# Performance work log

Measured on AMD Instinct MI355X. Metric: run time of the kernel, lower is better.

## Reference

```python
import jax
import jax.numpy as jnp
import numpy as np

ALPHA = 0.95
NUM_POS_FREQS = 4
CROSS_WEIGHT = 0.5
TOPK = 16
EPS = 1e-12


def _pos_enc(coords):
    # coords: [N, 4] -> [N, 4 * 2 * NUM_POS_FREQS]
    N = coords.shape[0]
    freqs = 2.0 ** jnp.arange(NUM_POS_FREQS, dtype=coords.dtype)  # [F]
    angles = coords[:, :, None] * (2.0 * jnp.pi) * freqs          # [N,4,F]
    pe = jnp.concatenate([jnp.sin(angles), jnp.cos(angles)], axis=-1)  # [N,4,2F]
    return pe.reshape(N, -1)


def _cosine_sim(x, y):
    # row-wise cosine similarity: [N,C] x [M,C] -> [N,M]
    xn = x / jnp.maximum(jnp.linalg.norm(x, axis=-1, keepdims=True), EPS)
    yn = y / jnp.maximum(jnp.linalg.norm(y, axis=-1, keepdims=True), EPS)
    return xn @ yn.T


def _sparsify_topk(A, k):
    # row-wise top-k, self-loop always kept (diag forced to max before top-k)
    N = A.shape[0]
    diag = jnp.arange(N)
    A_with_self = A.at[diag, diag].set(jnp.finfo(A.dtype).max)
    _, topk_idx = jax.lax.top_k(A_with_self, k)                   # [N,k]
    mask = jnp.zeros(A.shape, dtype=bool).at[diag[:, None], topk_idx].set(True)
    return jnp.where(mask, A, jnp.zeros((), A.dtype))


def _sym_normalize(A):
    deg = jnp.clip(A.sum(axis=-1, keepdims=True), EPS, None)      # [N,1]
    d_inv_sqrt = deg ** -0.5
    return d_inv_sqrt * A * d_inv_sqrt.T


def _build_adjacency(features, coordinates, history_features, history_coords):
    B, C = features.shape
    n, K, _ = history_features.shape
    H = n * K

    cur_feats = features
    cur_pos = _pos_enc(coordinates)
    A_cur = ALPHA * _cosine_sim(cur_feats, cur_feats) + (1.0 - ALPHA) * _cosine_sim(cur_pos, cur_pos)

    hist_feats = history_features.reshape(H, C)
    hist_pos = _pos_enc(history_coords.reshape(H, 4))
    A_hist = ALPHA * _cosine_sim(hist_feats, hist_feats) + (1.0 - ALPHA) * _cosine_sim(hist_pos, hist_pos)

    A_cross = ALPHA * _cosine_sim(cur_feats, hist_feats) + (1.0 - ALPHA) * _cosine_sim(cur_pos, hist_pos)
    A_cross = CROSS_WEIGHT * A_cross

    A = jnp.block([[A_cur, A_cross], [A_cross.T, A_hist]])        # [N,N], N=B+H
    node_feats = jnp.concatenate([cur_feats, hist_feats], axis=0)

    N = A.shape[0]
    if TOPK is not None and TOPK < N:
        A = _sparsify_topk(A, TOPK)
    A = _sym_normalize(A)
    return A[None], node_feats[None]


def setup_inputs() -> dict:
    key = jax.random.key(0)
    k1, k2, k3, k4 = jax.random.split(key, 4)
    B, C, n, K = 4096, 256, 128, 32
    return {
        "features": jax.random.normal(k1, (B, C), dtype=jnp.float32),
        "coordinates": jax.random.uniform(k2, (B, 4), dtype=jnp.float32),
        "history_features": jax.random.normal(k3, (n, K, C), dtype=jnp.float32),
        "history_coords": jax.random.uniform(k4, (n, K, 4), dtype=jnp.float32),
    }


def reference(features, coordinates, history_features, history_coords):
    adj, node_feats = _build_adjacency(features, coordinates, history_features, history_coords)
    return adj, node_feats
```

## Files before the change

### kernel.cpp

```cpp
#include <hip/hip_runtime.h>
#include <math.h>

#define B_CUR 4096
#define N_TOT 8192
#define C_F   256
#define C_TOT 288
#define KSEL  16

typedef unsigned short u16;
typedef __attribute__((ext_vector_type(8))) short short8;
typedef __attribute__((ext_vector_type(4))) float floatx4;

__device__ inline float bf2f(u16 v) {
  union { unsigned int u; float f; } x; x.u = ((unsigned int)v) << 16; return x.f;
}
__device__ inline u16 f2bf(float f) {
  union { float f; unsigned int u; } x; x.f = f;
  unsigned int u = x.u;
  u += ((u >> 16) & 1u) + 0x7FFFu;
  return (u16)(u >> 16);
}

#define GLD_LDS16(g, l) __builtin_amdgcn_global_load_lds(                      \
    (const __attribute__((address_space(1))) unsigned int*)(g),                \
    (__attribute__((address_space(3))) unsigned int*)(l), 16, 0, 0)

__global__ __launch_bounds__(256) void k_prep_feats(
    const float* __restrict__ feats, const float* __restrict__ hfeats,
    u16* __restrict__ Zb, float* __restrict__ out_nf) {
  int wave = threadIdx.x >> 6;
  int lane = threadIdx.x & 63;
  int row  = blockIdx.x * 4 + wave;
  const float* src = (row < B_CUR) ? (feats + (size_t)row * C_F)
                                   : (hfeats + (size_t)(row - B_CUR) * C_F);
  int c0 = lane * 4;
  float4 raw = *(const float4*)(src + c0);
  float ss = raw.x*raw.x + raw.y*raw.y + raw.z*raw.z + raw.w*raw.w;
  #pragma unroll
  for (int m = 32; m; m >>= 1) ss += __shfl_xor(ss, m, 64);
  float scale = 0.97467943448089633f / fmaxf(sqrtf(ss), 1e-12f);
  ushort4 o;
  o.x = f2bf(raw.x*scale); o.y = f2bf(raw.y*scale);
  o.z = f2bf(raw.z*scale); o.w = f2bf(raw.w*scale);
  *(ushort4*)(Zb + (size_t)row * C_TOT + c0) = o;
  *(float4*)(out_nf + (size_t)row * C_F + c0) = raw;
}

__global__ void k_prep_pos(const float* __restrict__ coords,
                           const float* __restrict__ hcoords,
                           u16* __restrict__ Zb) {
  int r = blockIdx.x * blockDim.x + threadIdx.x;
  if (r >= N_TOT) return;
  const float* src = (r < B_CUR) ? (coords + (size_t)r * 4)
                                 : (hcoords + (size_t)(r - B_CUR) * 4);
  float pe[32];
  float ss = 0.f;
  #pragma unroll
  for (int d = 0; d < 4; ++d) {
    float base = src[d] * 6.283185307179586f;
    #pragma unroll
    for (int f = 0; f < 4; ++f) {
      float ang = base * (float)(1 << f);
      float s = sinf(ang), co = cosf(ang);
      pe[d*8 + f]     = s;
      pe[d*8 + 4 + f] = co;
      ss += s*s + co*co;
    }
  }
  float scale = 0.22360679774997896f / fmaxf(sqrtf(ss), 1e-12f);
  u16* dst = Zb + (size_t)r * C_TOT + C_F;
  #pragma unroll
  for (int k = 0; k < 32; ++k) dst[k] = f2bf(pe[k] * scale);
}

#define EP_STRIDE 136
__global__ __launch_bounds__(256) void k_gemm_mfma(const u16* __restrict__ Zb,
                                                   u16* __restrict__ adj16) {
  __shared__ __align__(16) u16 smem[128 * EP_STRIDE];
  u16* As = smem;
  u16* Bs = smem + 4096;
  int tid  = threadIdx.x;
  int bi   = blockIdx.y, bj = blockIdx.x;
  int wave = tid >> 6, lane = tid & 63;
  int quad = lane >> 4, l16 = lane & 15;
  int m0w  = (wave >> 1) * 64;
  int n0w  = (wave & 1) * 64;
  int i0   = bi * 128, j0 = bj * 128;

  floatx4 acc[4][4];
  #pragma unroll
  for (int a = 0; a < 4; ++a)
    #pragma unroll
    for (int b = 0; b < 4; ++b) acc[a][b] = (floatx4){0.f, 0.f, 0.f, 0.f};

  int srow = wave * 16 + (lane >> 2);
  int sseg = (lane & 3) * 8;
  for (int kt = 0; kt < C_TOT; kt += 32) {
    #pragma unroll
    for (int it = 0; it < 2; ++it) {
      int row = it * 64 + srow;
      const u16* ga = Zb + (size_t)(i0 + row) * C_TOT + kt + sseg;
      const u16* gb = Zb + (size_t)(j0 + row) * C_TOT + kt + sseg;
      GLD_LDS16(ga, As + (it * 64 + wave * 16) * 32 + lane * 8);
      GLD_LDS16(gb, Bs + (it * 64 + wave * 16) * 32 + lane * 8);
    }
    __builtin_amdgcn_s_waitcnt(0);
    __syncthreads();
    short8 af[4], bf[4];
    #pragma unroll
    for (int mi = 0; mi < 4; ++mi)
      af[mi] = *(const short8*)(&As[(m0w + mi*16 + l16) * 32 + quad * 8]);
    #pragma unroll
    for (int ni = 0; ni < 4; ++ni)
      bf[ni] = *(const short8*)(&Bs[(n0w + ni*16 + l16) * 32 + quad * 8]);
    #pragma unroll
    for (int mi = 0; mi < 4; ++mi)
      #pragma unroll
      for (int ni = 0; ni < 4; ++ni)
        acc[mi][ni] = __builtin_amdgcn_mfma_f32_16x16x32_bf16(
            af[mi], bf[ni], acc[mi][ni], 0, 0, 0);
    __syncthreads();
  }

  float w = ((bi < 32) != (bj < 32)) ? 0.5f : 1.0f;
  #pragma unroll
  for (int mi = 0; mi < 4; ++mi) {
    #pragma unroll
    for (int ni = 0; ni < 4; ++ni) {
      int col = n0w + ni * 16 + l16;
      #pragma unroll
      for (int rg = 0; rg < 4; ++rg) {
        int row = m0w + mi * 16 + quad * 4 + rg;
        smem[row * EP_STRIDE + col] = f2bf(acc[mi][ni][rg] * w);
      }
    }
  }
  __syncthreads();
  #pragma unroll
  for (int it = 0; it < 8; ++it) {
    int idx = it * 256 + tid;
    int row = idx >> 4, l = idx & 15;
    uint4 v = *(const uint4*)(&smem[row * EP_STRIDE + l * 8]);
    *(uint4*)(&adj16[(size_t)(i0 + row) * 16384 + j0 + l * 8]) = v;
  }
}

#define TOP2(x) { unsigned int xv_ = (x); \
  if (xv_ > m1) { m2 = m1; m1 = xv_; } else if (xv_ > m2) { m2 = xv_; } }

__global__ __launch_bounds__(256) void k_topk(
    const u16* __restrict__ adj16,
    int* __restrict__ topk_idx, float* __restrict__ topk_val,
    float* __restrict__ deg_out) {
  __shared__ unsigned int keys[N_TOT];
  __shared__ unsigned int cand[64];
  __shared__ float s_diag;
  int r = blockIdx.x;
  int t = threadIdx.x;
  int wave = t >> 6, lane = t & 63;
  const u16* rowp = adj16 + (size_t)r * 16384;

  #pragma unroll
  for (int it = 0; it < 4; ++it) {
    int c0 = it * 2048 + t * 8;
    uint4 v = *(const uint4*)(rowp + c0);
    u16 e[8]; *(uint4*)e = v;
    unsigned int kk[8];
    #pragma unroll
    for (int q = 0; q < 8; ++q) {
      unsigned int b = e[q];
      unsigned int s16 = (b & 0x8000u) ? (b ^ 0xFFFFu) : (b | 0x8000u);
      kk[q] = (s16 << 16) | (unsigned int)(8191 - (c0 + q));
    }
    *(uint4*)(&keys[c0])     = *(uint4*)(&kk[0]);
    *(uint4*)(&keys[c0 + 4]) = *(uint4*)(&kk[4]);
  }
  __syncthreads();
  if (t == 0) {
    s_diag = bf2f(rowp[r]);
    keys[r] = 0xFFFF0000u | (unsigned int)(8191 - r);
  }
  __syncthreads();
  float diagval = s_diag;

  unsigned int m1 = 0, m2 = 0;
  int base = wave * 2048 + lane * 4;
  #pragma unroll
  for (int j = 0; j < 8; ++j) {
    uint4 v = *(const uint4*)(&keys[base + j * 256]);
    TOP2(v.x) TOP2(v.y) TOP2(v.z) TOP2(v.w)
  }

  for (int it = 0; it < KSEL; ++it) {
    unsigned int wmax = m1;
    #pragma unroll
    for (int s = 32; s; s >>= 1) {
      unsigned int o = (unsigned int)__shfl_xor((int)wmax, s, 64);
      wmax = (o > wmax) ? o : wmax;
    }
    if (lane == it) cand[wave * 16 + it] = wmax;
    if (m1 == wmax) {
      int col = 8191 - (int)(wmax & 0x1FFFu);
      keys[col] = 0;
      if (m2 != 0) { m1 = m2; m2 = 0; }
      else {
        m1 = 0; m2 = 0;
        #pragma unroll
        for (int j = 0; j < 8; ++j) {
          uint4 v = *(const uint4*)(&keys[base + j * 256]);
          TOP2(v.x) TOP2(v.y) TOP2(v.z) TOP2(v.w)
        }
      }
    }
  }
  __syncthreads();

  if (wave == 0) {
    unsigned int c = cand[lane];
    unsigned int myWin = 0;
    for (int it = 0; it < KSEL; ++it) {
      unsigned int wmax = c;
      #pragma unroll
      for (int s = 32; s; s >>= 1) {
        unsigned int o = (unsigned int)__shfl_xor((int)wmax, s, 64);
        wmax = (o > wmax) ? o : wmax;
      }
      if (c == wmax) c = 0;
      if (lane == it) myWin = wmax;
    }
    float val = 0.f;
    int col = 0;
    if (lane < KSEL) {
      unsigned int p = myWin;
      col = 8191 - (int)(p & 0x1FFFu);
      unsigned int k16 = p >> 16;
      unsigned int b = (k16 & 0x8000u) ? (k16 ^ 0x8000u) : ((~k16) & 0xFFFFu);
      val = (col == r) ? diagval : bf2f((u16)b);
      topk_idx[r * KSEL + lane] = col;
      topk_val[r * KSEL + lane] = val;
    }
    float s = (lane < KSEL) ? val : 0.f;
    #pragma unroll
    for (int m = 8; m; m >>= 1) s += __shfl_xor(s, m, 64);
    if (lane == 0) deg_out[r] = s;
  }
}

__global__ __launch_bounds__(256) void k_scale_zero(
    float* __restrict__ adj, const int* __restrict__ topk_idx,
    const float* __restrict__ topk_val, const float* __restrict__ deg) {
  int r = blockIdx.x, t = threadIdx.x;
  float* row = adj + (size_t)r * N_TOT;
  const float4 z4 = make_float4(0.f, 0.f, 0.f, 0.f);
  #pragma unroll
  for (int kk = 0; kk < 8; ++kk)
    *(float4*)(row + kk * 1024 + t * 4) = z4;
  __syncthreads();
  if (t < KSEL) {
    int j = topk_idx[r * KSEL + t];
    if (j < 0) j = 0; if (j >= N_TOT) j = N_TOT - 1;
    float v = topk_val[r * KSEL + t];
    float di = 1.0f / sqrtf(fmaxf(deg[r], 1e-12f));
    float dj = 1.0f / sqrtf(fmaxf(deg[j], 1e-12f));
    row[j] = v * di * dj;
  }
}

extern "C" void kernel_launch(void* const* d_in, const int* in_sizes, int n_in,
                              void* d_out, int out_size, void* d_ws, size_t ws_size,
                              hipStream_t stream) {
  const float* feats   = (const float*)d_in[0];
  const float* coords  = (const float*)d_in[1];
  const float* hfeats  = (const float*)d_in[2];
  const float* hcoords = (const float*)d_in[3];
  float* out    = (float*)d_out;
  float* adj    = out;
  u16*   adj16  = (u16*)out;
  float* out_nf = out + (size_t)N_TOT * N_TOT;

  char* ws    = (char*)d_ws;
  u16*  Zb    = (u16*)ws;
  size_t zb   = (size_t)N_TOT * C_TOT * sizeof(u16);
  zb = (zb + 255) & ~(size_t)255;
  int*   t_idx = (int*)(ws + zb);
  float* t_val = (float*)(ws + zb + (size_t)N_TOT*KSEL*sizeof(int));
  float* deg   = (float*)(ws + zb + (size_t)N_TOT*KSEL*(sizeof(int)+sizeof(float)));

  hipLaunchKernelGGL(k_prep_feats, dim3(N_TOT/4), dim3(256), 0, stream,
                     feats, hfeats, Zb, out_nf);
  hipLaunchKernelGGL(k_prep_pos, dim3(N_TOT/256), dim3(256), 0, stream,
                     coords, hcoords, Zb);
  hipLaunchKernelGGL(k_gemm_mfma, dim3(64, 64), dim3(256), 0, stream, Zb, adj16);
  hipLaunchKernelGGL(k_topk, dim3(N_TOT), dim3(256), 0, stream,
                     adj16, t_idx, t_val, deg);
  hipLaunchKernelGGL(k_scale_zero, dim3(N_TOT), dim3(256), 0, stream,
                     adj, t_idx, t_val, deg);
}
```

Measured before the change: 436.9 us.

## Exploit symmetry in Gram GEMM and widen K-tile to 96

The GEMM now launches only upper-triangular 128x128 tiles, decoding the tile index with a sqrt-based formula, and writes each off-diagonal tile twice, once directly and once transposed through shared memory. This roughly halves the MFMA work and the operand loads, since the similarity matrix is symmetric. The K loop also stages 96 columns per iteration instead of 32, cutting barrier and waitcnt round-trips at the cost of more LDS per block (48KB). Extra costs are a second epilogue pass with a column-major LDS write, which may hit bank conflicts, and uneven grid sizing.

```diff
diff --git a/kernel.cpp b/kernel.cpp
--- a/kernel.cpp
+++ b/kernel.cpp
@@ -6,6 +6,7 @@
 #define C_F   256
 #define C_TOT 288
 #define KSEL  16
+#define NTILE 64
 
 typedef unsigned short u16;
 typedef __attribute__((ext_vector_type(8))) short short8;
@@ -76,11 +77,19 @@
 #define EP_STRIDE 136
 __global__ __launch_bounds__(256) void k_gemm_mfma(const u16* __restrict__ Zb,
                                                    u16* __restrict__ adj16) {
-  __shared__ __align__(16) u16 smem[128 * EP_STRIDE];
+  __shared__ __align__(16) u16 smem[2 * 128 * 96];
   u16* As = smem;
-  u16* Bs = smem + 4096;
+  u16* Bs = smem + 128 * 96;
   int tid  = threadIdx.x;
-  int bi   = blockIdx.y, bj = blockIdx.x;
+
+  int t = blockIdx.x;
+  int bi = (int)floorf(((2.0f*NTILE + 1.0f) -
+            sqrtf((float)((2*NTILE+1)*(2*NTILE+1)) - 8.0f*(float)t)) * 0.5f);
+  if (bi < 0) bi = 0; if (bi > NTILE-1) bi = NTILE-1;
+  while (bi > 0 && t < bi*NTILE - bi*(bi-1)/2) --bi;
+  while (bi < NTILE-1 && t >= (bi+1)*NTILE - (bi+1)*bi/2) ++bi;
+  int bj = bi + (t - (bi*NTILE - bi*(bi-1)/2));
+
   int wave = tid >> 6, lane = tid & 63;
   int quad = lane >> 4, l16 = lane & 15;
   int m0w  = (wave >> 1) * 64;
@@ -93,36 +102,39 @@
     #pragma unroll
     for (int b = 0; b < 4; ++b) acc[a][b] = (floatx4){0.f, 0.f, 0.f, 0.f};
 
-  int srow = wave * 16 + (lane >> 2);
-  int sseg = (lane & 3) * 8;
-  for (int kt = 0; kt < C_TOT; kt += 32) {
-    #pragma unroll
-    for (int it = 0; it < 2; ++it) {
-      int row = it * 64 + srow;
-      const u16* ga = Zb + (size_t)(i0 + row) * C_TOT + kt + sseg;
-      const u16* gb = Zb + (size_t)(j0 + row) * C_TOT + kt + sseg;
-      GLD_LDS16(ga, As + (it * 64 + wave * 16) * 32 + lane * 8);
-      GLD_LDS16(gb, Bs + (it * 64 + wave * 16) * 32 + lane * 8);
+  for (int kt = 0; kt < C_TOT; kt += 96) {
+    #pragma unroll
+    for (int it = 0; it < 6; ++it) {
+      int s   = it * 256 + tid;
+      int row = s / 12, seg = s % 12;
+      const u16* ga = Zb + (size_t)(i0 + row) * C_TOT + kt + seg * 8;
+      const u16* gb = Zb + (size_t)(j0 + row) * C_TOT + kt + seg * 8;
+      GLD_LDS16(ga, As + s * 8);
+      GLD_LDS16(gb, Bs + s * 8);
     }
     __builtin_amdgcn_s_waitcnt(0);
     __syncthreads();
-    short8 af[4], bf[4];
-    #pragma unroll
-    for (int mi = 0; mi < 4; ++mi)
-      af[mi] = *(const short8*)(&As[(m0w + mi*16 + l16) * 32 + quad * 8]);
-    #pragma unroll
-    for (int ni = 0; ni < 4; ++ni)
-      bf[ni] = *(const short8*)(&Bs[(n0w + ni*16 + l16) * 32 + quad * 8]);
-    #pragma unroll
-    for (int mi = 0; mi < 4; ++mi)
+    #pragma unroll
+    for (int ks = 0; ks < 3; ++ks) {
+      short8 af[4], bf[4];
+      #pragma unroll
+      for (int mi = 0; mi < 4; ++mi)
+        af[mi] = *(const short8*)(&As[(m0w + mi*16 + l16) * 96 + ks*32 + quad*8]);
       #pragma unroll
       for (int ni = 0; ni < 4; ++ni)
-        acc[mi][ni] = __builtin_amdgcn_mfma_f32_16x16x32_bf16(
-            af[mi], bf[ni], acc[mi][ni], 0, 0, 0);
+        bf[ni] = *(const short8*)(&Bs[(n0w + ni*16 + l16) * 96 + ks*32 + quad*8]);
+      #pragma unroll
+      for (int mi = 0; mi < 4; ++mi)
+        #pragma unroll
+        for (int ni = 0; ni < 4; ++ni)
+          acc[mi][ni] = __builtin_amdgcn_mfma_f32_16x16x32_bf16(
+              af[mi], bf[ni], acc[mi][ni], 0, 0, 0);
+    }
     __syncthreads();
   }
 
   float w = ((bi < 32) != (bj < 32)) ? 0.5f : 1.0f;
+
   #pragma unroll
   for (int mi = 0; mi < 4; ++mi) {
     #pragma unroll
@@ -142,6 +154,30 @@
     int row = idx >> 4, l = idx & 15;
     uint4 v = *(const uint4*)(&smem[row * EP_STRIDE + l * 8]);
     *(uint4*)(&adj16[(size_t)(i0 + row) * 16384 + j0 + l * 8]) = v;
+  }
+
+  if (bi != bj) {
+    __syncthreads();
+    #pragma unroll
+    for (int mi = 0; mi < 4; ++mi) {
+      #pragma unroll
+      for (int ni = 0; ni < 4; ++ni) {
+        int col = n0w + ni * 16 + l16;
+        #pragma unroll
+        for (int rg = 0; rg < 4; ++rg) {
+          int row = m0w + mi * 16 + quad * 4 + rg;
+          smem[col * EP_STRIDE + row] = f2bf(acc[mi][ni][rg] * w);
+        }
+      }
+    }
+    __syncthreads();
+    #pragma unroll
+    for (int it = 0; it < 8; ++it) {
+      int idx = it * 256 + tid;
+      int row = idx >> 4, l = idx & 15;
+      uint4 v = *(const uint4*)(&smem[row * EP_STRIDE + l * 8]);
+      *(uint4*)(&adj16[(size_t)(j0 + row) * 16384 + i0 + l * 8]) = v;
+    }
   }
 }
 
@@ -290,7 +326,8 @@
                      feats, hfeats, Zb, out_nf);
   hipLaunchKernelGGL(k_prep_pos, dim3(N_TOT/256), dim3(256), 0, stream,
                      coords, hcoords, Zb);
-  hipLaunchKernelGGL(k_gemm_mfma, dim3(64, 64), dim3(256), 0, stream, Zb, adj16);
+  hipLaunchKernelGGL(k_gemm_mfma, dim3(NTILE*(NTILE+1)/2), dim3(256), 0, stream,
+                     Zb, adj16);
   hipLaunchKernelGGL(k_topk, dim3(N_TOT), dim3(256), 0, stream,
                      adj16, t_idx, t_val, deg);
   hipLaunchKernelGGL(k_scale_zero, dim3(N_TOT), dim3(256), 0, stream,
```

Measured after the change: 431.8 us. About the same (-1.2%).
